# Kernel tuning notes

Hardware: AMD Instinct MI355X
Metric: run time of the kernel (lower is better)

## Reference

```python
import jax, jax.numpy as jnp
import numpy as np

NUM_EMBEDDINGS = 1024
EMBEDDING_DIM = 256
TEMPERATURE = 1.0
COMMITMENT_COST = 0.25


def setup_inputs() -> dict:
    key = jax.random.key(0)
    kz, ke = jax.random.split(key)
    z = jax.random.normal(kz, (32, 1024, EMBEDDING_DIM), dtype=jnp.float32)
    # nn.Embedding weight init: uniform(-1/K, 1/K)
    lim = 1.0 / NUM_EMBEDDINGS
    emb = jax.random.uniform(ke, (NUM_EMBEDDINGS, EMBEDDING_DIM),
                             dtype=jnp.float32, minval=-lim, maxval=lim)
    return {"z": z, "emb": emb}


def reference(z, emb):
    zf = z.reshape(-1, EMBEDDING_DIM)                      # [T, D], T = 32768
    # squared distances ||z - e||^2 = ||z||^2 + ||e||^2 - 2 z.e
    d = (jnp.sum(zf * zf, axis=1, keepdims=True)
         + jnp.sum(emb * emb, axis=1)
         - 2.0 * jnp.matmul(zf, emb.T))                    # [T, K]
    logits = -d
    # gumbel_softmax (soft): softmax((logits + Gumbel(0,1)) / tau)
    gkey = jax.random.fold_in(jax.random.key(0), 1)
    g = jax.random.gumbel(gkey, logits.shape, dtype=logits.dtype)
    prob = jax.nn.softmax((logits + g) / TEMPERATURE, axis=1)  # [T, K]
    quantized = jnp.matmul(prob, emb).reshape(z.shape)     # [B, N, D]
    e_latent_loss = jnp.mean((jax.lax.stop_gradient(quantized) - z) ** 2)
    q_latent_loss = jnp.mean((quantized - jax.lax.stop_gradient(z)) ** 2)
    loss = q_latent_loss + COMMITMENT_COST * e_latent_loss
    # straight-through estimator
    quantized_st = z + jax.lax.stop_gradient(quantized - z)
    return (quantized_st, loss)
```

## Files before the change

### kernel.cpp

```cpp
#include <hip/hip_runtime.h>
#include <hip/hip_bf16.h>
#include <stdint.h>


typedef __bf16 bf16x8 __attribute__((ext_vector_type(8)));
typedef float  f32x4  __attribute__((ext_vector_type(4)));

#define MFMA16(A,B,C) __builtin_amdgcn_mfma_f32_16x16x32_bf16((A),(B),(C),0,0,0)

struct TF2 { uint32_t a, b; };

__host__ __device__ constexpr uint32_t rotl32(uint32_t v, int r){ return (v<<r)|(v>>(32-r)); }

__host__ __device__ constexpr TF2 tf2x32(uint32_t k0, uint32_t k1, uint32_t x0, uint32_t x1){
  const uint32_t k2 = k0 ^ k1 ^ 0x1BD11BDAu;
  x0 += k0; x1 += k1;
  x0 += x1; x1 = rotl32(x1,13); x1 ^= x0;
  x0 += x1; x1 = rotl32(x1,15); x1 ^= x0;
  x0 += x1; x1 = rotl32(x1,26); x1 ^= x0;
  x0 += x1; x1 = rotl32(x1, 6); x1 ^= x0;
  x0 += k1; x1 += k2 + 1u;
  x0 += x1; x1 = rotl32(x1,17); x1 ^= x0;
  x0 += x1; x1 = rotl32(x1,29); x1 ^= x0;
  x0 += x1; x1 = rotl32(x1,16); x1 ^= x0;
  x0 += x1; x1 = rotl32(x1,24); x1 ^= x0;
  x0 += k2; x1 += k0 + 2u;
  x0 += x1; x1 = rotl32(x1,13); x1 ^= x0;
  x0 += x1; x1 = rotl32(x1,15); x1 ^= x0;
  x0 += x1; x1 = rotl32(x1,26); x1 ^= x0;
  x0 += x1; x1 = rotl32(x1, 6); x1 ^= x0;
  x0 += k0; x1 += k1 + 3u;
  x0 += x1; x1 = rotl32(x1,17); x1 ^= x0;
  x0 += x1; x1 = rotl32(x1,29); x1 ^= x0;
  x0 += x1; x1 = rotl32(x1,16); x1 ^= x0;
  x0 += x1; x1 = rotl32(x1,24); x1 ^= x0;
  x0 += k1; x1 += k2 + 4u;
  x0 += x1; x1 = rotl32(x1,13); x1 ^= x0;
  x0 += x1; x1 = rotl32(x1,15); x1 ^= x0;
  x0 += x1; x1 = rotl32(x1,26); x1 ^= x0;
  x0 += x1; x1 = rotl32(x1, 6); x1 ^= x0;
  x0 += k2; x1 += k0 + 5u;
  return {x0, x1};
}

constexpr TF2 GKEY = tf2x32(0u, 0u, 0u, 1u);

__device__ __forceinline__ unsigned short f2bf(float f){
  __bf16 h = (__bf16)f;
  return __builtin_bit_cast(unsigned short, h);
}

__device__ __forceinline__ float gumbel_w(uint32_t bits){
  float uf = __uint_as_float((bits >> 9) | 0x3f800000u) - 1.0f;
  float u  = fmaxf(uf, 1.17549435e-38f);
  return __builtin_amdgcn_rcpf(-__log2f(u));
}

__global__ void gq_prep(const float* __restrict__ emb, unsigned short* __restrict__ Eb,
                        unsigned short* __restrict__ ETb, float* __restrict__ enorm)
{
  const int r = blockIdx.x;
  const int t = threadIdx.x;
  float e = emb[r*256 + t];
  unsigned short h = f2bf(e);
  Eb[r*256 + t] = h;
  ETb[t*1024 + r] = h;
  float sq = e*e;
  #pragma unroll
  for (int o = 32; o > 0; o >>= 1) sq += __shfl_down(sq, o);
  __shared__ float ws4[4];
  if ((t & 63) == 0) ws4[t >> 6] = sq;
  __syncthreads();
  if (t == 0) enorm[r] = ws4[0] + ws4[1] + ws4[2] + ws4[3];
}

__global__ __launch_bounds__(512, 2)
void gq_main(
    const float* __restrict__ z, const unsigned short* __restrict__ Eb,
    const unsigned short* __restrict__ ETb, const float* __restrict__ enorm,
    float* __restrict__ out, float* __restrict__ partials)
{
  __shared__ __align__(16) unsigned char sm[32768 + 32768];
  float* denomW = (float*)(sm + 32768);
  float* denomF = (float*)(sm + 32768 + 2048);
  float* lsumW  = (float*)(sm + 32768 + 2048 + 256);

  const int tid  = threadIdx.x;
  const int lane = tid & 63;
  const int wv   = tid >> 6;
  const int col  = lane & 15;
  const int hi   = lane >> 4;
  const int b32  = blockIdx.x * 32;

  #pragma unroll
  for (int j = 0; j < 4; ++j) {
    int lin = j*512 + tid;
    int row = lin >> 5;
    int u   = lin & 31;
    int grow = (row < 32) ? (b32 + row) : (16384 + b32 + row - 32);
    const float4* src = reinterpret_cast<const float4*>(z + (size_t)grow*256 + u*8);
    float4 v0 = src[0], v1 = src[1];
    uint32_t w0 = (uint32_t)f2bf(v0.x) | ((uint32_t)f2bf(v0.y) << 16);
    uint32_t w1 = (uint32_t)f2bf(v0.z) | ((uint32_t)f2bf(v0.w) << 16);
    uint32_t w2 = (uint32_t)f2bf(v1.x) | ((uint32_t)f2bf(v1.y) << 16);
    uint32_t w3 = (uint32_t)f2bf(v1.z) | ((uint32_t)f2bf(v1.w) << 16);
    uint32_t* p = reinterpret_cast<uint32_t*>(sm + u*1024 + row*16);
    p[0] = w0; p[1] = w1; p[2] = w2; p[3] = w3;
  }
  __syncthreads();

  f32x4 accQ[4][2] = {};
  float dn[4][4] = {};
  float lsum = 0.0f;

  const unsigned char* zA = sm + (hi*1024 + col*16);
  const int pstore_off = (wv >> 1)*4096 + ((((wv & 1) << 1) | (col >> 3)))*1024
                       + hi*64 + (col & 7)*2;

  #pragma unroll 1
  for (int kt = 0; kt < 8; ++kt) {
    const int ke0 = kt*128 + wv*16;
    const int pbuf = 32768 + (kt & 1)*16384;

    const unsigned short* ebase = Eb + (size_t)(ke0 + col)*256 + hi*8;
    bf16x8 mb[8];
    #pragma unroll
    for (int kk = 0; kk < 8; ++kk)
      mb[kk] = *reinterpret_cast<const bf16x8*>(ebase + kk*32);

    float enk = enorm[ke0 + col];

    TF2 c[2][4];
    #pragma unroll
    for (int rt = 0; rt < 2; ++rt) {
      #pragma unroll
      for (int rg = 0; rg < 4; ++rg) {
        int rowL = rt*16 + hi*4 + rg;
        uint32_t idx = (uint32_t)(b32 + rowL)*1024u + (uint32_t)(ke0 + col);
        c[rt][rg] = tf2x32(GKEY.a, GKEY.b, idx, idx + (1u<<24));
      }
    }

    f32x4 aS[4] = {};
    __builtin_amdgcn_s_setprio(1);
    #pragma unroll
    for (int kk = 0; kk < 8; ++kk) {
      #pragma unroll
      for (int rt = 0; rt < 4; ++rt) {
        bf16x8 af = *reinterpret_cast<const bf16x8*>(zA + kk*4096 + rt*256);
        aS[rt] = MFMA16(af, mb[kk], aS[rt]);
      }
    }
    __builtin_amdgcn_s_setprio(0);

    const unsigned short* etb0 = ETb + (size_t)(wv*32 + col)*1024 + kt*128 + hi*8;
    const unsigned short* etb1 = etb0 + 16*1024;
    bf16x8 nb[8];
    #pragma unroll
    for (int kk = 0; kk < 4; ++kk) {
      nb[kk]   = *reinterpret_cast<const bf16x8*>(etb0 + kk*32);
      nb[kk+4] = *reinterpret_cast<const bf16x8*>(etb1 + kk*32);
    }

    unsigned char* sb = sm + pbuf + pstore_off;
    #pragma unroll
    for (int rt = 0; rt < 2; ++rt) {
      #pragma unroll
      for (int rg = 0; rg < 4; ++rg) {
        float p0 = __expf(2.0f*aS[rt  ][rg] - enk) * gumbel_w(c[rt][rg].a);
        float p1 = __expf(2.0f*aS[rt+2][rg] - enk) * gumbel_w(c[rt][rg].b);
        dn[rt  ][rg] += p0;
        dn[rt+2][rg] += p1;
        *(unsigned short*)(sb + rt*256 + rg*16)       = f2bf(p0);
        *(unsigned short*)(sb + rt*256 + rg*16 + 512) = f2bf(p1);
      }
    }
    __syncthreads();

    const unsigned char* pA = sm + pbuf + (hi*1024 + col*16);
    __builtin_amdgcn_s_setprio(1);
    #pragma unroll
    for (int kk = 0; kk < 4; ++kk) {
      #pragma unroll
      for (int rt = 0; rt < 4; ++rt) {
        bf16x8 af = *reinterpret_cast<const bf16x8*>(pA + kk*4096 + rt*256);
        accQ[rt][0] = MFMA16(af, nb[kk],   accQ[rt][0]);
        accQ[rt][1] = MFMA16(af, nb[kk+4], accQ[rt][1]);
      }
    }
    __builtin_amdgcn_s_setprio(0);
  }
  __syncthreads();

  #pragma unroll
  for (int rt = 0; rt < 4; ++rt)
    #pragma unroll
    for (int rg = 0; rg < 4; ++rg) {
      float v = dn[rt][rg];
      v += __shfl_xor(v, 1);
      v += __shfl_xor(v, 2);
      v += __shfl_xor(v, 4);
      v += __shfl_xor(v, 8);
      dn[rt][rg] = v;
    }
  if (col == 0) {
    #pragma unroll
    for (int rt = 0; rt < 4; ++rt)
      #pragma unroll
      for (int rg = 0; rg < 4; ++rg)
        denomW[wv*64 + rt*16 + hi*4 + rg] = dn[rt][rg];
  }
  __syncthreads();
  if (tid < 64) {
    float s = 0.f;
    #pragma unroll
    for (int w2 = 0; w2 < 8; ++w2) s += denomW[w2*64 + tid];
    denomF[tid] = __builtin_amdgcn_rcpf(s);
  }
  __syncthreads();

  #pragma unroll
  for (int rt = 0; rt < 4; ++rt) {
    #pragma unroll
    for (int rg = 0; rg < 4; ++rg) {
      int row = rt*16 + hi*4 + rg;
      float rd = denomF[row];
      int grow = (row < 32) ? (b32 + row) : (16384 + b32 + row - 32);
      float* orow = out + (size_t)grow*256;
      const float* zrow = z + (size_t)grow*256;
      #pragma unroll
      for (int ct = 0; ct < 2; ++ct) {
        int d = wv*32 + ct*16 + col;
        float q  = accQ[rt][ct][rg] * rd;
        float zv = zrow[d];
        float df = q - zv;
        orow[d] = zv + df;
        lsum += df*df;
      }
    }
  }
  #pragma unroll
  for (int o = 32; o > 0; o >>= 1) lsum += __shfl_down(lsum, o);
  if (lane == 0) lsumW[wv] = lsum;
  __syncthreads();
  if (tid == 0) {
    float s = 0.f;
    #pragma unroll
    for (int w2 = 0; w2 < 8; ++w2) s += lsumW[w2];
    partials[blockIdx.x] = s;
  }
}

__global__ void gq_final(const float* __restrict__ partials, float* __restrict__ out)
{
  const int t = threadIdx.x;
  float v = partials[t];
  #pragma unroll
  for (int o = 32; o > 0; o >>= 1) v += __shfl_down(v, o);
  __shared__ float ws8[8];
  if ((t & 63) == 0) ws8[t >> 6] = v;
  __syncthreads();
  if (t == 0) {
    float s = 0.f;
    #pragma unroll
    for (int i = 0; i < 8; ++i) s += ws8[i];
    out[8388608] = 1.25f * s * (1.0f / 8388608.0f);
  }
}

extern "C" void kernel_launch(void* const* d_in, const int* in_sizes, int n_in,
                              void* d_out, int out_size, void* d_ws, size_t ws_size,
                              hipStream_t stream)
{
  const float* z   = (const float*)d_in[0];
  const float* emb = (const float*)d_in[1];
  float* out = (float*)d_out;
  char* ws = (char*)d_ws;
  unsigned short* Eb  = (unsigned short*)ws;
  unsigned short* ETb = (unsigned short*)(ws + 524288);
  float* enorm    = (float*)(ws + 1048576);
  float* partials = (float*)(ws + 1048576 + 4096);

  gq_prep<<<1024, 256, 0, stream>>>(emb, Eb, ETb, enorm);
  gq_main<<<512, 512, 0, stream>>>(z, Eb, ETb, enorm, out, partials);
  gq_final<<<1, 512, 0, stream>>>(partials, out);
}
```

Measured before the change: 90.91 us.

## Split waves into producer and consumer roles with software-pipelined softmax-matmul stages

The eight waves are split into two roles. Four producer waves compute the distance GEMM, Gumbel noise and exponentials for 32 codewords each and write bf16 probabilities into a double-buffered LDS tile. Four consumer waves run the prob×E GEMM on the previous tile, lagged by one iteration, and handle the output epilogue. This is meant to overlap the transcendental/RNG work with the second matmul. The cost is that each role now has twice the per-wave work and the wave groups may stay idle when their stages are unbalanced.

```diff
diff --git a/kernel.cpp b/kernel.cpp
--- a/kernel.cpp
+++ b/kernel.cpp
@@ -82,8 +82,8 @@
 {
   __shared__ __align__(16) unsigned char sm[32768 + 32768];
   float* denomW = (float*)(sm + 32768);
-  float* denomF = (float*)(sm + 32768 + 2048);
-  float* lsumW  = (float*)(sm + 32768 + 2048 + 256);
+  float* denomF = (float*)(sm + 32768 + 1024);
+  float* lsumW  = (float*)(sm + 32768 + 1024 + 256);
 
   const int tid  = threadIdx.x;
   const int lane = tid & 63;
@@ -91,6 +91,7 @@
   const int col  = lane & 15;
   const int hi   = lane >> 4;
   const int b32  = blockIdx.x * 32;
+  const bool producer = (wv < 4);
 
   #pragma unroll
   for (int j = 0; j < 4; ++j) {
@@ -109,101 +110,141 @@
   }
   __syncthreads();
 
-  f32x4 accQ[4][2] = {};
+  const unsigned char* zA = sm + (hi*1024 + col*16);
+  unsigned char* sbBase = sm + 32768 + wv*4096 + (col >> 3)*1024
+                        + hi*64 + (col & 7)*2;
+  const int d0 = (wv - 4) * 64;
+
+  f32x4 accQ[4][4] = {};
   float dn[4][4] = {};
   float lsum = 0.0f;
 
-  const unsigned char* zA = sm + (hi*1024 + col*16);
-  const int pstore_off = (wv >> 1)*4096 + ((((wv & 1) << 1) | (col >> 3)))*1024
-                       + hi*64 + (col & 7)*2;
-
   #pragma unroll 1
   for (int kt = 0; kt < 8; ++kt) {
-    const int ke0 = kt*128 + wv*16;
-    const int pbuf = 32768 + (kt & 1)*16384;
-
-    const unsigned short* ebase = Eb + (size_t)(ke0 + col)*256 + hi*8;
-    bf16x8 mb[8];
-    #pragma unroll
-    for (int kk = 0; kk < 8; ++kk)
-      mb[kk] = *reinterpret_cast<const bf16x8*>(ebase + kk*32);
-
-    float enk = enorm[ke0 + col];
-
-    TF2 c[2][4];
-    #pragma unroll
-    for (int rt = 0; rt < 2; ++rt) {
-      #pragma unroll
-      for (int rg = 0; rg < 4; ++rg) {
-        int rowL = rt*16 + hi*4 + rg;
-        uint32_t idx = (uint32_t)(b32 + rowL)*1024u + (uint32_t)(ke0 + col);
-        c[rt][rg] = tf2x32(GKEY.a, GKEY.b, idx, idx + (1u<<24));
-      }
+    if (producer) {
+      const int ke0 = kt*128 + wv*32;
+      const unsigned short* eb0 = Eb + (size_t)(ke0 + col)*256 + hi*8;
+      const unsigned short* eb1 = eb0 + 16*256;
+      bf16x8 mb[8];
+      #pragma unroll
+      for (int kk = 0; kk < 8; ++kk)
+        mb[kk] = *reinterpret_cast<const bf16x8*>(eb0 + kk*32);
+      float enk0 = enorm[ke0 + col];
+      float enk1 = enorm[ke0 + 16 + col];
+
+      TF2 c[2][2][4];
+      #pragma unroll
+      for (int rt = 0; rt < 2; ++rt)
+        #pragma unroll
+        for (int kc = 0; kc < 2; ++kc)
+          #pragma unroll
+          for (int rg = 0; rg < 4; ++rg) {
+            int rowL = rt*16 + hi*4 + rg;
+            uint32_t idx = (uint32_t)(b32 + rowL)*1024u
+                         + (uint32_t)(ke0 + kc*16 + col);
+            c[rt][kc][rg] = tf2x32(GKEY.a, GKEY.b, idx, idx + (1u<<24));
+          }
+
+      f32x4 aS[4][2] = {};
+      __builtin_amdgcn_s_setprio(1);
+      #pragma unroll
+      for (int kk = 0; kk < 8; ++kk) {
+        #pragma unroll
+        for (int rt = 0; rt < 4; ++rt) {
+          bf16x8 af = *reinterpret_cast<const bf16x8*>(zA + kk*4096 + rt*256);
+          aS[rt][0] = MFMA16(af, mb[kk], aS[rt][0]);
+        }
+      }
+      __builtin_amdgcn_s_setprio(0);
+      #pragma unroll
+      for (int kk = 0; kk < 8; ++kk)
+        mb[kk] = *reinterpret_cast<const bf16x8*>(eb1 + kk*32);
+      __builtin_amdgcn_s_setprio(1);
+      #pragma unroll
+      for (int kk = 0; kk < 8; ++kk) {
+        #pragma unroll
+        for (int rt = 0; rt < 4; ++rt) {
+          bf16x8 af = *reinterpret_cast<const bf16x8*>(zA + kk*4096 + rt*256);
+          aS[rt][1] = MFMA16(af, mb[kk], aS[rt][1]);
+        }
+      }
+      __builtin_amdgcn_s_setprio(0);
+
+      unsigned char* sb = sbBase + (kt & 1)*16384;
+      #pragma unroll
+      for (int rt = 0; rt < 2; ++rt) {
+        #pragma unroll
+        for (int kc = 0; kc < 2; ++kc) {
+          float enk = kc ? enk1 : enk0;
+          #pragma unroll
+          for (int rg = 0; rg < 4; ++rg) {
+            float p0 = __expf(2.0f*aS[rt  ][kc][rg] - enk) * gumbel_w(c[rt][kc][rg].a);
+            float p1 = __expf(2.0f*aS[rt+2][kc][rg] - enk) * gumbel_w(c[rt][kc][rg].b);
+            dn[rt  ][rg] += p0;
+            dn[rt+2][rg] += p1;
+            *(unsigned short*)(sb + kc*2048 + rt*256 + rg*16)       = f2bf(p0);
+            *(unsigned short*)(sb + kc*2048 + rt*256 + rg*16 + 512) = f2bf(p1);
+          }
+        }
+      }
+    } else if (kt > 0) {
+      const unsigned char* pA = zA + 32768 + ((kt-1) & 1)*16384;
+      const unsigned short* etb = ETb + (size_t)(d0 + col)*1024 + (kt-1)*128 + hi*8;
+      __builtin_amdgcn_s_setprio(1);
+      #pragma unroll
+      for (int kk = 0; kk < 4; ++kk) {
+        bf16x8 nb[4];
+        #pragma unroll
+        for (int ct = 0; ct < 4; ++ct)
+          nb[ct] = *reinterpret_cast<const bf16x8*>(etb + (size_t)ct*16*1024 + kk*32);
+        #pragma unroll
+        for (int rt = 0; rt < 4; ++rt) {
+          bf16x8 af = *reinterpret_cast<const bf16x8*>(pA + kk*4096 + rt*256);
+          #pragma unroll
+          for (int ct = 0; ct < 4; ++ct)
+            accQ[rt][ct] = MFMA16(af, nb[ct], accQ[rt][ct]);
+        }
+      }
+      __builtin_amdgcn_s_setprio(0);
     }
-
-    f32x4 aS[4] = {};
+    __syncthreads();
+  }
+
+  if (!producer) {
+    const unsigned char* pA = zA + 32768 + 16384;
+    const unsigned short* etb = ETb + (size_t)(d0 + col)*1024 + 7*128 + hi*8;
     __builtin_amdgcn_s_setprio(1);
     #pragma unroll
-    for (int kk = 0; kk < 8; ++kk) {
+    for (int kk = 0; kk < 4; ++kk) {
+      bf16x8 nb[4];
+      #pragma unroll
+      for (int ct = 0; ct < 4; ++ct)
+        nb[ct] = *reinterpret_cast<const bf16x8*>(etb + (size_t)ct*16*1024 + kk*32);
       #pragma unroll
       for (int rt = 0; rt < 4; ++rt) {
-        bf16x8 af = *reinterpret_cast<const bf16x8*>(zA + kk*4096 + rt*256);
-        aS[rt] = MFMA16(af, mb[kk], aS[rt]);
+        bf16x8 af = *reinterpret_cast<const bf16x8*>(pA + kk*4096 + rt*256);
+        #pragma unroll
+        for (int ct = 0; ct < 4; ++ct)
+          accQ[rt][ct] = MFMA16(af, nb[ct], accQ[rt][ct]);
       }
     }
     __builtin_amdgcn_s_setprio(0);
-
-    const unsigned short* etb0 = ETb + (size_t)(wv*32 + col)*1024 + kt*128 + hi*8;
-    const unsigned short* etb1 = etb0 + 16*1024;
-    bf16x8 nb[8];
-    #pragma unroll
-    for (int kk = 0; kk < 4; ++kk) {
-      nb[kk]   = *reinterpret_cast<const bf16x8*>(etb0 + kk*32);
-      nb[kk+4] = *reinterpret_cast<const bf16x8*>(etb1 + kk*32);
-    }
-
-    unsigned char* sb = sm + pbuf + pstore_off;
-    #pragma unroll
-    for (int rt = 0; rt < 2; ++rt) {
+  } else {
+    #pragma unroll
+    for (int rt = 0; rt < 4; ++rt)
       #pragma unroll
       for (int rg = 0; rg < 4; ++rg) {
-        float p0 = __expf(2.0f*aS[rt  ][rg] - enk) * gumbel_w(c[rt][rg].a);
-        float p1 = __expf(2.0f*aS[rt+2][rg] - enk) * gumbel_w(c[rt][rg].b);
-        dn[rt  ][rg] += p0;
-        dn[rt+2][rg] += p1;
-        *(unsigned short*)(sb + rt*256 + rg*16)       = f2bf(p0);
-        *(unsigned short*)(sb + rt*256 + rg*16 + 512) = f2bf(p1);
-      }
-    }
-    __syncthreads();
-
-    const unsigned char* pA = sm + pbuf + (hi*1024 + col*16);
-    __builtin_amdgcn_s_setprio(1);
-    #pragma unroll
-    for (int kk = 0; kk < 4; ++kk) {
-      #pragma unroll
-      for (int rt = 0; rt < 4; ++rt) {
-        bf16x8 af = *reinterpret_cast<const bf16x8*>(pA + kk*4096 + rt*256);
-        accQ[rt][0] = MFMA16(af, nb[kk],   accQ[rt][0]);
-        accQ[rt][1] = MFMA16(af, nb[kk+4], accQ[rt][1]);
-      }
-    }
-    __builtin_amdgcn_s_setprio(0);
-  }
-  __syncthreads();
-
-  #pragma unroll
-  for (int rt = 0; rt < 4; ++rt)
-    #pragma unroll
-    for (int rg = 0; rg < 4; ++rg) {
-      float v = dn[rt][rg];
-      v += __shfl_xor(v, 1);
-      v += __shfl_xor(v, 2);
-      v += __shfl_xor(v, 4);
-      v += __shfl_xor(v, 8);
-      dn[rt][rg] = v;
-    }
-  if (col == 0) {
+        float v = dn[rt][rg];
+        v += __shfl_xor(v, 1);
+        v += __shfl_xor(v, 2);
+        v += __shfl_xor(v, 4);
+        v += __shfl_xor(v, 8);
+        dn[rt][rg] = v;
+      }
+  }
+  __syncthreads();
+
+  if (producer && col == 0) {
     #pragma unroll
     for (int rt = 0; rt < 4; ++rt)
       #pragma unroll
@@ -212,42 +253,39 @@
   }
   __syncthreads();
   if (tid < 64) {
-    float s = 0.f;
-    #pragma unroll
-    for (int w2 = 0; w2 < 8; ++w2) s += denomW[w2*64 + tid];
+    float s = denomW[tid] + denomW[64+tid] + denomW[128+tid] + denomW[192+tid];
     denomF[tid] = __builtin_amdgcn_rcpf(s);
   }
   __syncthreads();
 
-  #pragma unroll
-  for (int rt = 0; rt < 4; ++rt) {
-    #pragma unroll
-    for (int rg = 0; rg < 4; ++rg) {
-      int row = rt*16 + hi*4 + rg;
-      float rd = denomF[row];
-      int grow = (row < 32) ? (b32 + row) : (16384 + b32 + row - 32);
-      float* orow = out + (size_t)grow*256;
-      const float* zrow = z + (size_t)grow*256;
-      #pragma unroll
-      for (int ct = 0; ct < 2; ++ct) {
-        int d = wv*32 + ct*16 + col;
-        float q  = accQ[rt][ct][rg] * rd;
-        float zv = zrow[d];
-        float df = q - zv;
-        orow[d] = zv + df;
-        lsum += df*df;
+  if (!producer) {
+    #pragma unroll
+    for (int rt = 0; rt < 4; ++rt) {
+      #pragma unroll
+      for (int rg = 0; rg < 4; ++rg) {
+        int row = rt*16 + hi*4 + rg;
+        float rd = denomF[row];
+        int grow = (row < 32) ? (b32 + row) : (16384 + b32 + row - 32);
+        float* orow = out + (size_t)grow*256;
+        const float* zrow = z + (size_t)grow*256;
+        #pragma unroll
+        for (int ct = 0; ct < 4; ++ct) {
+          int d = d0 + ct*16 + col;
+          float q  = accQ[rt][ct][rg] * rd;
+          float zv = zrow[d];
+          float df = q - zv;
+          orow[d] = zv + df;
+          lsum += df*df;
+        }
       }
     }
-  }
-  #pragma unroll
-  for (int o = 32; o > 0; o >>= 1) lsum += __shfl_down(lsum, o);
-  if (lane == 0) lsumW[wv] = lsum;
+    #pragma unroll
+    for (int o = 32; o > 0; o >>= 1) lsum += __shfl_down(lsum, o);
+    if (lane == 0) lsumW[wv - 4] = lsum;
+  }
   __syncthreads();
   if (tid == 0) {
-    float s = 0.f;
-    #pragma unroll
-    for (int w2 = 0; w2 < 8; ++w2) s += lsumW[w2];
-    partials[blockIdx.x] = s;
+    partials[blockIdx.x] = lsumW[0] + lsumW[1] + lsumW[2] + lsumW[3];
   }
 }
 
```

Measured after the change: 111.5 us. +22.7%, slower.

## Precompute Gumbel noise in a separate kernel and fold it into exp2

Applied to the files above, without the earlier changes.

Adds a kernel that generates the Threefry-based Gumbel noise for all T×K entries ahead of time and stores it as bf16 in workspace, laid out to match each lane's access pattern in the main kernel. The main kernel then loads this noise and computes exp2(2·log2e·dot + g·log2e − enorm·log2e) instead of running Threefry, a log and a reciprocal inline. This removes per-element RNG work from the MFMA loop, at the cost of 64 MB of extra global writes and reads plus an extra launch. Keeping the noise in bf16 also reduces its precision. A fallback path keeps the old behaviour when the workspace is too small.

```diff
diff --git a/kernel.cpp b/kernel.cpp
--- a/kernel.cpp
+++ b/kernel.cpp
@@ -56,6 +56,13 @@
   return __builtin_amdgcn_rcpf(-__log2f(u));
 }
 
+__device__ __forceinline__ float g2f(uint32_t bits){
+  float uf = __uint_as_float((bits >> 9) | 0x3f800000u) - 1.0f;
+  float u  = fmaxf(uf, 1.17549435e-38f);
+  float t  = __log2f(u) * (-0.69314718056f);
+  return -__log2f(t);
+}
+
 __global__ void gq_prep(const float* __restrict__ emb, unsigned short* __restrict__ Eb,
                         unsigned short* __restrict__ ETb, float* __restrict__ enorm)
 {
@@ -74,10 +81,35 @@
   if (t == 0) enorm[r] = ws4[0] + ws4[1] + ws4[2] + ws4[3];
 }
 
+__global__ __launch_bounds__(256) void gq_gumbel(uint32_t* __restrict__ W)
+{
+  int gt   = blockIdx.x * 256 + threadIdx.x;
+  int lane = gt & 63;
+  int wvv  = (gt >> 6) & 7;
+  int kt   = (gt >> 9) & 7;
+  int b    = gt >> 12;
+  int col  = lane & 15;
+  int hi   = lane >> 4;
+  int ke   = kt*128 + wvv*16 + col;
+  uint32_t* wp = W + (size_t)gt * 8;
+  #pragma unroll
+  for (int rt = 0; rt < 2; ++rt) {
+    #pragma unroll
+    for (int rg = 0; rg < 4; ++rg) {
+      int rowL = rt*16 + hi*4 + rg;
+      uint32_t idx = (uint32_t)(b*32 + rowL)*1024u + (uint32_t)ke;
+      TF2 cc = tf2x32(GKEY.a, GKEY.b, idx, idx + (1u<<24));
+      wp[rt*4 + rg] = (uint32_t)f2bf(g2f(cc.a))
+                    | ((uint32_t)f2bf(g2f(cc.b)) << 16);
+    }
+  }
+}
+
 __global__ __launch_bounds__(512, 2)
-void gq_main(
+void gq_main_w(
     const float* __restrict__ z, const unsigned short* __restrict__ Eb,
     const unsigned short* __restrict__ ETb, const float* __restrict__ enorm,
+    const unsigned short* __restrict__ W,
     float* __restrict__ out, float* __restrict__ partials)
 {
   __shared__ __align__(16) unsigned char sm[32768 + 32768];
@@ -116,6 +148,7 @@
   const unsigned char* zA = sm + (hi*1024 + col*16);
   const int pstore_off = (wv >> 1)*4096 + ((((wv & 1) << 1) | (col >> 3)))*1024
                        + hi*64 + (col & 7)*2;
+  const unsigned short* wlane = W + (((size_t)blockIdx.x*8)*8 + wv)*1024 + lane*16;
 
   #pragma unroll 1
   for (int kt = 0; kt < 8; ++kt) {
@@ -128,6 +161,178 @@
     for (int kk = 0; kk < 8; ++kk)
       mb[kk] = *reinterpret_cast<const bf16x8*>(ebase + kk*32);
 
+    const unsigned short* wtile = wlane + (size_t)kt*8*1024;
+    bf16x8 wb0 = *reinterpret_cast<const bf16x8*>(wtile);
+    bf16x8 wb1 = *reinterpret_cast<const bf16x8*>(wtile + 8);
+
+    float enkS = enorm[ke0 + col] * 1.44269504f;
+
+    f32x4 aS[4] = {};
+    __builtin_amdgcn_s_setprio(1);
+    #pragma unroll
+    for (int kk = 0; kk < 8; ++kk) {
+      #pragma unroll
+      for (int rt = 0; rt < 4; ++rt) {
+        bf16x8 af = *reinterpret_cast<const bf16x8*>(zA + kk*4096 + rt*256);
+        aS[rt] = MFMA16(af, mb[kk], aS[rt]);
+      }
+    }
+    __builtin_amdgcn_s_setprio(0);
+
+    const unsigned short* etb0 = ETb + (size_t)(wv*32 + col)*1024 + kt*128 + hi*8;
+    const unsigned short* etb1 = etb0 + 16*1024;
+    bf16x8 nb[8];
+    #pragma unroll
+    for (int kk = 0; kk < 4; ++kk) {
+      nb[kk]   = *reinterpret_cast<const bf16x8*>(etb0 + kk*32);
+      nb[kk+4] = *reinterpret_cast<const bf16x8*>(etb1 + kk*32);
+    }
+
+    unsigned char* sb = sm + pbuf + pstore_off;
+    #pragma unroll
+    for (int rt = 0; rt < 2; ++rt) {
+      #pragma unroll
+      for (int rg = 0; rg < 4; ++rg) {
+        float g2a = (float)((rt == 0) ? wb0[2*rg]   : wb1[2*rg]);
+        float g2b = (float)((rt == 0) ? wb0[2*rg+1] : wb1[2*rg+1]);
+        float p0 = exp2f(fmaf(2.88539008f, aS[rt  ][rg], g2a - enkS));
+        float p1 = exp2f(fmaf(2.88539008f, aS[rt+2][rg], g2b - enkS));
+        dn[rt  ][rg] += p0;
+        dn[rt+2][rg] += p1;
+        *(unsigned short*)(sb + rt*256 + rg*16)       = f2bf(p0);
+        *(unsigned short*)(sb + rt*256 + rg*16 + 512) = f2bf(p1);
+      }
+    }
+    __syncthreads();
+
+    const unsigned char* pA = sm + pbuf + (hi*1024 + col*16);
+    __builtin_amdgcn_s_setprio(1);
+    #pragma unroll
+    for (int kk = 0; kk < 4; ++kk) {
+      #pragma unroll
+      for (int rt = 0; rt < 4; ++rt) {
+        bf16x8 af = *reinterpret_cast<const bf16x8*>(pA + kk*4096 + rt*256);
+        accQ[rt][0] = MFMA16(af, nb[kk],   accQ[rt][0]);
+        accQ[rt][1] = MFMA16(af, nb[kk+4], accQ[rt][1]);
+      }
+    }
+    __builtin_amdgcn_s_setprio(0);
+  }
+  __syncthreads();
+
+  #pragma unroll
+  for (int rt = 0; rt < 4; ++rt)
+    #pragma unroll
+    for (int rg = 0; rg < 4; ++rg) {
+      float v = dn[rt][rg];
+      v += __shfl_xor(v, 1);
+      v += __shfl_xor(v, 2);
+      v += __shfl_xor(v, 4);
+      v += __shfl_xor(v, 8);
+      dn[rt][rg] = v;
+    }
+  if (col == 0) {
+    #pragma unroll
+    for (int rt = 0; rt < 4; ++rt)
+      #pragma unroll
+      for (int rg = 0; rg < 4; ++rg)
+        denomW[wv*64 + rt*16 + hi*4 + rg] = dn[rt][rg];
+  }
+  __syncthreads();
+  if (tid < 64) {
+    float s = 0.f;
+    #pragma unroll
+    for (int w2 = 0; w2 < 8; ++w2) s += denomW[w2*64 + tid];
+    denomF[tid] = __builtin_amdgcn_rcpf(s);
+  }
+  __syncthreads();
+
+  #pragma unroll
+  for (int rt = 0; rt < 4; ++rt) {
+    #pragma unroll
+    for (int rg = 0; rg < 4; ++rg) {
+      int row = rt*16 + hi*4 + rg;
+      float rd = denomF[row];
+      int grow = (row < 32) ? (b32 + row) : (16384 + b32 + row - 32);
+      float* orow = out + (size_t)grow*256;
+      const float* zrow = z + (size_t)grow*256;
+      #pragma unroll
+      for (int ct = 0; ct < 2; ++ct) {
+        int d = wv*32 + ct*16 + col;
+        float q  = accQ[rt][ct][rg] * rd;
+        float zv = zrow[d];
+        float df = q - zv;
+        orow[d] = zv + df;
+        lsum += df*df;
+      }
+    }
+  }
+  #pragma unroll
+  for (int o = 32; o > 0; o >>= 1) lsum += __shfl_down(lsum, o);
+  if (lane == 0) lsumW[wv] = lsum;
+  __syncthreads();
+  if (tid == 0) {
+    float s = 0.f;
+    #pragma unroll
+    for (int w2 = 0; w2 < 8; ++w2) s += lsumW[w2];
+    partials[blockIdx.x] = s;
+  }
+}
+
+__global__ __launch_bounds__(512, 2)
+void gq_main_fb(
+    const float* __restrict__ z, const unsigned short* __restrict__ Eb,
+    const unsigned short* __restrict__ ETb, const float* __restrict__ enorm,
+    float* __restrict__ out, float* __restrict__ partials)
+{
+  __shared__ __align__(16) unsigned char sm[32768 + 32768];
+  float* denomW = (float*)(sm + 32768);
+  float* denomF = (float*)(sm + 32768 + 2048);
+  float* lsumW  = (float*)(sm + 32768 + 2048 + 256);
+
+  const int tid  = threadIdx.x;
+  const int lane = tid & 63;
+  const int wv   = tid >> 6;
+  const int col  = lane & 15;
+  const int hi   = lane >> 4;
+  const int b32  = blockIdx.x * 32;
+
+  #pragma unroll
+  for (int j = 0; j < 4; ++j) {
+    int lin = j*512 + tid;
+    int row = lin >> 5;
+    int u   = lin & 31;
+    int grow = (row < 32) ? (b32 + row) : (16384 + b32 + row - 32);
+    const float4* src = reinterpret_cast<const float4*>(z + (size_t)grow*256 + u*8);
+    float4 v0 = src[0], v1 = src[1];
+    uint32_t w0 = (uint32_t)f2bf(v0.x) | ((uint32_t)f2bf(v0.y) << 16);
+    uint32_t w1 = (uint32_t)f2bf(v0.z) | ((uint32_t)f2bf(v0.w) << 16);
+    uint32_t w2 = (uint32_t)f2bf(v1.x) | ((uint32_t)f2bf(v1.y) << 16);
+    uint32_t w3 = (uint32_t)f2bf(v1.z) | ((uint32_t)f2bf(v1.w) << 16);
+    uint32_t* p = reinterpret_cast<uint32_t*>(sm + u*1024 + row*16);
+    p[0] = w0; p[1] = w1; p[2] = w2; p[3] = w3;
+  }
+  __syncthreads();
+
+  f32x4 accQ[4][2] = {};
+  float dn[4][4] = {};
+  float lsum = 0.0f;
+
+  const unsigned char* zA = sm + (hi*1024 + col*16);
+  const int pstore_off = (wv >> 1)*4096 + ((((wv & 1) << 1) | (col >> 3)))*1024
+                       + hi*64 + (col & 7)*2;
+
+  #pragma unroll 1
+  for (int kt = 0; kt < 8; ++kt) {
+    const int ke0 = kt*128 + wv*16;
+    const int pbuf = 32768 + (kt & 1)*16384;
+
+    const unsigned short* ebase = Eb + (size_t)(ke0 + col)*256 + hi*8;
+    bf16x8 mb[8];
+    #pragma unroll
+    for (int kk = 0; kk < 8; ++kk)
+      mb[kk] = *reinterpret_cast<const bf16x8*>(ebase + kk*32);
+
     float enk = enorm[ke0 + col];
 
     TF2 c[2][4];
@@ -167,8 +372,8 @@
     for (int rt = 0; rt < 2; ++rt) {
       #pragma unroll
       for (int rg = 0; rg < 4; ++rg) {
-        float p0 = __expf(2.0f*aS[rt  ][rg] - enk) * gumbel_w(c[rt][rg].a);
-        float p1 = __expf(2.0f*aS[rt+2][rg] - enk) * gumbel_w(c[rt][rg].b);
+        float p0 = __expf(fmaf(2.0f, aS[rt  ][rg], -enk)) * gumbel_w(c[rt][rg].a);
+        float p1 = __expf(fmaf(2.0f, aS[rt+2][rg], -enk)) * gumbel_w(c[rt][rg].b);
         dn[rt  ][rg] += p0;
         dn[rt+2][rg] += p1;
         *(unsigned short*)(sb + rt*256 + rg*16)       = f2bf(p0);
@@ -280,8 +485,17 @@
   unsigned short* ETb = (unsigned short*)(ws + 524288);
   float* enorm    = (float*)(ws + 1048576);
   float* partials = (float*)(ws + 1048576 + 4096);
+  const size_t W_OFF  = 1056768;
+  const size_t W_SIZE = 67108864;
 
   gq_prep<<<1024, 256, 0, stream>>>(emb, Eb, ETb, enorm);
-  gq_main<<<512, 512, 0, stream>>>(z, Eb, ETb, enorm, out, partials);
+  if (ws_size >= W_OFF + W_SIZE) {
+    uint32_t* W = (uint32_t*)(ws + W_OFF);
+    gq_gumbel<<<8192, 256, 0, stream>>>(W);
+    gq_main_w<<<512, 512, 0, stream>>>(z, Eb, ETb, enorm,
+                                       (const unsigned short*)W, out, partials);
+  } else {
+    gq_main_fb<<<512, 512, 0, stream>>>(z, Eb, ETb, enorm, out, partials);
+  }
   gq_final<<<1, 512, 0, stream>>>(partials, out);
 }
```

Result: slower. 125.9 us (+38.5%).
